# Optimization experiments

Hardware: AMD Instinct MI355X
Metric: run time of the kernel (lower is better)

The kernel has to match this reference:

```python
import jax, jax.numpy as jnp
import numpy as np

N, IN_DIM, HEADS, OUT_DIM = 4096, 128, 4, 64
NEG_INF = -9.0e15  # finite mask value, matches torch source


def setup_inputs() -> dict:
    key = jax.random.key(0)
    k1, k2, k3, k4, k5 = jax.random.split(key, 5)
    x = jax.random.normal(k1, (N, IN_DIM), dtype=jnp.float32)
    adj_mask = jax.random.bernoulli(k2, 0.1, (N, N))  # bool, j->i edges
    # xavier-uniform-ish scales
    lim_w = float(np.sqrt(6.0 / (IN_DIM + HEADS * OUT_DIM)))
    W_lin = jax.random.uniform(k3, (IN_DIM, HEADS * OUT_DIM), minval=-lim_w, maxval=lim_w, dtype=jnp.float32)
    lim_a = float(np.sqrt(6.0 / (2 * OUT_DIM + 1)))
    a_src = jax.random.uniform(k4, (OUT_DIM,), minval=-lim_a, maxval=lim_a, dtype=jnp.float32)
    a_dst = jax.random.uniform(k5, (OUT_DIM,), minval=-lim_a, maxval=lim_a, dtype=jnp.float32)
    return {"x": x, "adj_mask": adj_mask, "W_lin": W_lin, "a_src": a_src, "a_dst": a_dst}


def reference(x, adj_mask, W_lin, a_src, a_dst):
    n = x.shape[0]
    h = (x @ W_lin).reshape(n, HEADS, OUT_DIM)           # (N, H, D)
    # att(cat(h_i, h_j)) decomposes linearly: a_src.h_i + a_dst.h_j
    s_i = jnp.einsum("nhd,d->nh", h, a_src)              # (N, H) contribution of dest node i
    s_j = jnp.einsum("nhd,d->nh", h, a_dst)              # (N, H) contribution of source node j
    e = jax.nn.leaky_relu(s_i[:, None, :] + s_j[None, :, :], 0.2)  # (N, N, H)
    e = jnp.where(adj_mask[:, :, None], e, NEG_INF)
    attn = jax.nn.softmax(e, axis=1)                     # softmax over source nodes j
    out = jnp.einsum("ijh,jhd->ihd", attn, h)            # per-head aggregation
    return out.reshape(n, HEADS * OUT_DIM)               # concat=True
```

## Files before the change

### kernel.cpp

```cpp
#include <hip/hip_runtime.h>
#include <math.h>


#define N 4096
#define IN_DIM 128
#define HEADS 4
#define OUT_DIM 64
#define HD 256
#define LOG2E 1.4426950408889634f

typedef _Float16 f16x8 __attribute__((ext_vector_type(8)));
typedef __fp16 fp16x2 __attribute__((ext_vector_type(2)));
typedef float f32x4 __attribute__((ext_vector_type(4)));

union F16x8u { fp16x2 h2[4]; f16x8 v; };

#define WS_HB_OFF    0u
#define WS_SSRC_OFF  2097152u
#define WS_SDST_OFF  2162688u
#define WS_SDT_OFF   2228224u
#define WS_L2L_OFF   2293760u
#define WS_U_OFF     2359296u
#define WS_BITS_OFF  2424832u
#define WS_BITT_OFF  4521984u
#define WS_PART_OFF  6619136u
#define WS_NEEDED    (6619136u + 33554432u)

__device__ __forceinline__ float f4get(float4 v, int h) {
  return h == 0 ? v.x : h == 1 ? v.y : h == 2 ? v.z : v.w;
}
__device__ __forceinline__ float lrelu(float v) { return fmaxf(v, 0.2f * v); }

__device__ __forceinline__ unsigned pack_bytes(unsigned v) {
  return (v & 1u) | ((v >> 7) & 2u) | ((v >> 14) & 4u) | ((v >> 21) & 8u);
}

__global__ __launch_bounds__(256) void pack_mask_k(const void* __restrict__ mraw,
                                                   unsigned* __restrict__ bits,
                                                   unsigned* __restrict__ bits_t) {
  __shared__ int s_flag;
  if (threadIdx.x == 0) s_flag = 0;
  __syncthreads();
  const unsigned* mw = (const unsigned*)mraw;
  int bad = 0, g = 0;
  for (int i = threadIdx.x; i < 1024; i += 256) {
    unsigned v = mw[i];
    if (v & 0xFEFEFEFEu) bad = 1;
    if (v > 1u) g = 1;
  }
  if (bad || g) atomicOr(&s_flag, (bad ? 1 : 0) | (g ? 2 : 0));
  __syncthreads();
  const bool byte_fmt = ((s_flag & 1) == 0) && ((s_flag & 2) != 0);

  int w = blockIdx.x * blockDim.x + threadIdx.x;
  unsigned ob = 0u;
  if (byte_fmt) {
    const uint4* p = (const uint4*)((const unsigned char*)mraw + (size_t)w * 32u);
    uint4 a = p[0], b = p[1];
    ob  =  pack_bytes(a.x)        | (pack_bytes(a.y) << 4)  | (pack_bytes(a.z) << 8)  | (pack_bytes(a.w) << 12);
    ob |= (pack_bytes(b.x) << 16) | (pack_bytes(b.y) << 20) | (pack_bytes(b.z) << 24) | (pack_bytes(b.w) << 28);
  } else {
    const uint4* p = (const uint4*)((const unsigned*)mraw + (size_t)w * 32u);
#pragma unroll
    for (int k = 0; k < 8; ++k) {
      uint4 v = p[k];
      ob |= (v.x ? 1u : 0u) << (4 * k);
      ob |= (v.y ? 1u : 0u) << (4 * k + 1);
      ob |= (v.z ? 1u : 0u) << (4 * k + 2);
      ob |= (v.w ? 1u : 0u) << (4 * k + 3);
    }
  }
  bits[w] = ob;
  const int row = w >> 7, jc = w & 127;
  bits_t[((size_t)(row >> 6) * 128 + jc) * 64 + (row & 63)] = ob;
}

__global__ __launch_bounds__(256) void compute_h(const float* __restrict__ x,
                                                 const float* __restrict__ W,
                                                 const float* __restrict__ a_src,
                                                 const float* __restrict__ a_dst,
                                                 _Float16* __restrict__ hb,
                                                 float* __restrict__ s_src,
                                                 float* __restrict__ s_dst,
                                                 float* __restrict__ s_dst_t) {
  const int i0 = blockIdx.x * 8;
  const int c = threadIdx.x;

  float acc[8];
#pragma unroll
  for (int r = 0; r < 8; ++r) acc[r] = 0.f;

  for (int kk = 0; kk < IN_DIM / 4; ++kk) {
    const int k = kk * 4;
    float w0 = W[(size_t)(k + 0) * HD + c];
    float w1 = W[(size_t)(k + 1) * HD + c];
    float w2 = W[(size_t)(k + 2) * HD + c];
    float w3 = W[(size_t)(k + 3) * HD + c];
#pragma unroll
    for (int r = 0; r < 8; ++r) {
      float4 xv = *(const float4*)(x + (size_t)(i0 + r) * IN_DIM + k);
      acc[r] = fmaf(xv.x, w0, fmaf(xv.y, w1, fmaf(xv.z, w2, fmaf(xv.w, w3, acc[r]))));
    }
  }

  {
    const int head = c >> 6, nt = (c >> 4) & 3, m15 = c & 15;
    const int unit = (head * 128 + (i0 >> 5)) * 4 + nt;
    const int lanep = ((i0 & 31) >> 3) * 16 + m15;
    f16x8 v;
#pragma unroll
    for (int r = 0; r < 8; ++r) v[r] = (_Float16)acc[r];
    *(f16x8*)(hb + (size_t)unit * 512 + lanep * 8) = v;
  }

  const int hw = c >> 6, lane = c & 63;
  const float as = a_src[lane], ad = a_dst[lane];
#pragma unroll
  for (int r = 0; r < 8; ++r) {
    float vs = acc[r] * as, vd = acc[r] * ad;
#pragma unroll
    for (int off = 1; off < 64; off <<= 1) {
      vs += __shfl_xor(vs, off);
      vd += __shfl_xor(vd, off);
    }
    if (lane == 0) {
      s_src[(size_t)(i0 + r) * HEADS + hw] = vs * LOG2E;
      s_dst[(size_t)(i0 + r) * HEADS + hw] = vd * LOG2E;
      s_dst_t[(size_t)hw * N + (i0 + r)] = vd * LOG2E;
    }
  }
}

__global__ __launch_bounds__(256) void gat_scores(const float* __restrict__ s_src,
                                                  const float* __restrict__ s_dst,
                                                  const unsigned* __restrict__ bits,
                                                  float* __restrict__ log2l_ws,
                                                  float* __restrict__ U_ws) {
  const int tid = threadIdx.x;
  const int wave = tid >> 6;
  const int lane = tid & 63;
  const int row = blockIdx.x * 4 + wave;

  const float4* sd4 = (const float4*)s_dst;
  const unsigned long long* mb64 = (const unsigned long long*)bits + (size_t)row * 64;

  float4 siv = ((const float4*)s_src)[row];
  float si[4] = {siv.x, siv.y, siv.z, siv.w};
  float l[4] = {0.f, 0.f, 0.f, 0.f};

  for (int jb = 0; jb < N / 256; ++jb) {
    float4 sj[4];
    unsigned long long w[4];
#pragma unroll
    for (int u = 0; u < 4; ++u) {
      sj[u] = sd4[jb * 256 + u * 64 + lane];
      w[u] = mb64[jb * 4 + u];
    }
#pragma unroll
    for (int u = 0; u < 4; ++u) {
      bool e = (w[u] >> lane) & 1ull;
#pragma unroll
      for (int h = 0; h < 4; ++h) {
        float ev = __builtin_amdgcn_exp2f(lrelu(si[h] + f4get(sj[u], h)));
        l[h] += e ? ev : 0.f;
      }
    }
  }
#pragma unroll
  for (int off = 1; off < 64; off <<= 1)
#pragma unroll
    for (int h = 0; h < 4; ++h) l[h] += __shfl_xor(l[h], off);

  if (lane == 0) {
#pragma unroll
    for (int h = 0; h < 4; ++h) {
      bool empty = (l[h] == 0.f);
      log2l_ws[(size_t)row * HEADS + h] = empty ? 12.0f : __log2f(l[h]);
      U_ws[(size_t)row * HEADS + h] = empty ? 0.f : -1.0e38f;
    }
  }
}

__global__ __launch_bounds__(512, 4) void gat_aggr(const _Float16* __restrict__ hb,
                                                   const float* __restrict__ s_src,
                                                   const float* __restrict__ s_dst_t,
                                                   const float* __restrict__ log2l_ws,
                                                   const float* __restrict__ U_ws,
                                                   const unsigned* __restrict__ bits_t,
                                                   float* __restrict__ dst,
                                                   int atomic_mode) {
  const int tid = threadIdx.x;
  const int wave = tid >> 6;
  const int lane = tid & 63;
  const int head = wave & 3;
  const int mg = wave >> 2;
  const int m15 = lane & 15;
  const int quad = lane >> 4;
  const int jq = blockIdx.x & 7;
  const int it = blockIdx.x >> 3;
  const int i0 = it * 64;
  const int rA = i0 + mg * 32 + m15;
  const int rB = rA + 16;

  const float siA = s_src[(size_t)rA * HEADS + head];
  const float siB = s_src[(size_t)rB * HEADS + head];
  const float nlA = -log2l_ws[(size_t)rA * HEADS + head];
  const float nlB = -log2l_ws[(size_t)rB * HEADS + head];
  const float UA = U_ws[(size_t)rA * HEADS + head];
  const float UB = U_ws[(size_t)rB * HEADS + head];

  const unsigned* mt = bits_t + ((size_t)it * 128 + jq * 16) * 64 + mg * 32 + m15;
  const float* sjb = s_dst_t + (size_t)head * N + jq * 512 + quad * 8;
  const _Float16* hbp = hb + ((size_t)(head * 128 + jq * 16) * 4) * 512 + lane * 8;

  f32x4 accA0 = {0.f, 0.f, 0.f, 0.f}, accA1 = accA0, accA2 = accA0, accA3 = accA0;
  f32x4 accB0 = accA0, accB1 = accA0, accB2 = accA0, accB3 = accA0;

  const int shq = quad * 8;

  for (int c = 0; c < 16; ++c) {
    const unsigned mwA = mt[c * 64];
    const unsigned mwB = mt[c * 64 + 16];
    const float4 sa = *(const float4*)(sjb + c * 32);
    const float4 sb = *(const float4*)(sjb + c * 32 + 4);

    const f16x8 b0 = *(const f16x8*)(hbp + (size_t)(c * 4 + 0) * 512);
    const f16x8 b1 = *(const f16x8*)(hbp + (size_t)(c * 4 + 1) * 512);
    const f16x8 b2 = *(const f16x8*)(hbp + (size_t)(c * 4 + 2) * 512);
    const f16x8 b3 = *(const f16x8*)(hbp + (size_t)(c * 4 + 3) * 512);

    const unsigned wA = mwA >> shq;
    const unsigned wB = mwB >> shq;
    const float sjs[8] = {sa.x, sa.y, sa.z, sa.w, sb.x, sb.y, sb.z, sb.w};

    F16x8u uA, uB;
#pragma unroll
    for (int t2 = 0; t2 < 4; ++t2) {
      float pA[2], pB[2];
#pragma unroll
      for (int q = 0; q < 2; ++q) {
        const int t = t2 * 2 + q;
        const float sj = sjs[t];
        float vA = lrelu(siA + sj);
        float vB = lrelu(siB + sj);
        float xA = ((wA >> t) & 1u) ? vA : UA;
        float xB = ((wB >> t) & 1u) ? vB : UB;
        pA[q] = __builtin_amdgcn_exp2f(xA + nlA);
        pB[q] = __builtin_amdgcn_exp2f(xB + nlB);
      }
      uA.h2[t2] = __builtin_amdgcn_cvt_pkrtz(pA[0], pA[1]);
      uB.h2[t2] = __builtin_amdgcn_cvt_pkrtz(pB[0], pB[1]);
    }

    accA0 = __builtin_amdgcn_mfma_f32_16x16x32_f16(uA.v, b0, accA0, 0, 0, 0);
    accA1 = __builtin_amdgcn_mfma_f32_16x16x32_f16(uA.v, b1, accA1, 0, 0, 0);
    accA2 = __builtin_amdgcn_mfma_f32_16x16x32_f16(uA.v, b2, accA2, 0, 0, 0);
    accA3 = __builtin_amdgcn_mfma_f32_16x16x32_f16(uA.v, b3, accA3, 0, 0, 0);
    accB0 = __builtin_amdgcn_mfma_f32_16x16x32_f16(uB.v, b0, accB0, 0, 0, 0);
    accB1 = __builtin_amdgcn_mfma_f32_16x16x32_f16(uB.v, b1, accB1, 0, 0, 0);
    accB2 = __builtin_amdgcn_mfma_f32_16x16x32_f16(uB.v, b2, accB2, 0, 0, 0);
    accB3 = __builtin_amdgcn_mfma_f32_16x16x32_f16(uB.v, b3, accB3, 0, 0, 0);
  }

  const int colb = head * 64 + m15;
  if (atomic_mode) {
    float* oA = dst + (size_t)(i0 + mg * 32 + quad * 4) * HD + colb;
    float* oB = oA + (size_t)16 * HD;
#pragma unroll
    for (int reg = 0; reg < 4; ++reg) {
      atomicAdd(oA + (size_t)reg * HD + 0,  accA0[reg]);
      atomicAdd(oA + (size_t)reg * HD + 16, accA1[reg]);
      atomicAdd(oA + (size_t)reg * HD + 32, accA2[reg]);
      atomicAdd(oA + (size_t)reg * HD + 48, accA3[reg]);
      atomicAdd(oB + (size_t)reg * HD + 0,  accB0[reg]);
      atomicAdd(oB + (size_t)reg * HD + 16, accB1[reg]);
      atomicAdd(oB + (size_t)reg * HD + 32, accB2[reg]);
      atomicAdd(oB + (size_t)reg * HD + 48, accB3[reg]);
    }
  } else {
    float* oA = dst + (size_t)jq * (N * HD) + (size_t)(i0 + mg * 32 + quad * 4) * HD + colb;
    float* oB = oA + (size_t)16 * HD;
#pragma unroll
    for (int reg = 0; reg < 4; ++reg) {
      oA[(size_t)reg * HD + 0]  = accA0[reg];
      oA[(size_t)reg * HD + 16] = accA1[reg];
      oA[(size_t)reg * HD + 32] = accA2[reg];
      oA[(size_t)reg * HD + 48] = accA3[reg];
      oB[(size_t)reg * HD + 0]  = accB0[reg];
      oB[(size_t)reg * HD + 16] = accB1[reg];
      oB[(size_t)reg * HD + 32] = accB2[reg];
      oB[(size_t)reg * HD + 48] = accB3[reg];
    }
  }
}

__global__ __launch_bounds__(256) void reduce_part(const float4* __restrict__ part,
                                                   float4* __restrict__ out) {
  const size_t idx = (size_t)blockIdx.x * 256 + threadIdx.x;
  const size_t S = (size_t)N * HD / 4;
  float4 o = part[idx];
#pragma unroll
  for (int k = 1; k < 8; ++k) {
    float4 a = part[idx + (size_t)k * S];
    o.x += a.x; o.y += a.y; o.z += a.z; o.w += a.w;
  }
  out[idx] = o;
}

extern "C" void kernel_launch(void* const* d_in, const int* in_sizes, int n_in,
                              void* d_out, int out_size, void* d_ws, size_t ws_size,
                              hipStream_t stream) {
  (void)in_sizes; (void)n_in;
  const float* x = (const float*)d_in[0];
  const void* mask = d_in[1];
  const float* W = (const float*)d_in[2];
  const float* a_src = (const float*)d_in[3];
  const float* a_dst = (const float*)d_in[4];
  float* out = (float*)d_out;

  char* ws = (char*)d_ws;
  _Float16* hb = (_Float16*)(ws + WS_HB_OFF);
  float* s_src = (float*)(ws + WS_SSRC_OFF);
  float* s_dst = (float*)(ws + WS_SDST_OFF);
  float* s_dst_t = (float*)(ws + WS_SDT_OFF);
  float* log2l_ws = (float*)(ws + WS_L2L_OFF);
  float* U_ws = (float*)(ws + WS_U_OFF);
  unsigned* bits = (unsigned*)(ws + WS_BITS_OFF);
  unsigned* bits_t = (unsigned*)(ws + WS_BITT_OFF);
  float* partial = (float*)(ws + WS_PART_OFF);

  pack_mask_k<<<(N * N / 32) / 256, 256, 0, stream>>>(mask, bits, bits_t);
  compute_h<<<N / 8, 256, 0, stream>>>(x, W, a_src, a_dst, hb, s_src, s_dst, s_dst_t);
  gat_scores<<<N / 4, 256, 0, stream>>>(s_src, s_dst, bits, log2l_ws, U_ws);

  if (ws_size >= (size_t)WS_NEEDED) {
    gat_aggr<<<(N / 64) * 8, 512, 0, stream>>>(hb, s_src, s_dst_t, log2l_ws, U_ws,
                                               bits_t, partial, 0);
    reduce_part<<<(N * HD / 4) / 256, 256, 0, stream>>>((const float4*)partial, (float4*)out);
  } else {
    (void)hipMemsetAsync(out, 0, (size_t)out_size * sizeof(float), stream);
    gat_aggr<<<(N / 64) * 8, 512, 0, stream>>>(hb, s_src, s_dst_t, log2l_ws, U_ws,
                                               bits_t, out, 1);
  }
}
```

Baseline: 174.0 us.

## Drop separate softmax-denominator pass using fixed shift and deferred normalization

Removes the gat_scores kernel that computed per-row softmax denominators, instead accumulating the denominator inside the aggregation loop with a constant exponent shift and normalizing in the reduce step. It also merges mask packing and the h projection into one launch, drops the row-major mask bit array, and adds a fallback for empty rows using the column mean of h. This saves a full pass over the mask and the score exponentials, at the cost of extra per-element adds and a fixed shift that could overflow or underflow fp16 if scores span a wide range.

```diff
diff --git a/kernel.cpp b/kernel.cpp
--- a/kernel.cpp
+++ b/kernel.cpp
@@ -8,6 +8,7 @@
 #define OUT_DIM 64
 #define HD 256
 #define LOG2E 1.4426950408889634f
+#define PSHIFT 8.0f
 
 typedef _Float16 f16x8 __attribute__((ext_vector_type(8)));
 typedef __fp16 fp16x2 __attribute__((ext_vector_type(2)));
@@ -17,166 +18,117 @@
 
 #define WS_HB_OFF    0u
 #define WS_SSRC_OFF  2097152u
-#define WS_SDST_OFF  2162688u
-#define WS_SDT_OFF   2228224u
-#define WS_L2L_OFF   2293760u
-#define WS_U_OFF     2359296u
-#define WS_BITS_OFF  2424832u
-#define WS_BITT_OFF  4521984u
-#define WS_PART_OFF  6619136u
-#define WS_NEEDED    (6619136u + 33554432u)
-
-__device__ __forceinline__ float f4get(float4 v, int h) {
-  return h == 0 ? v.x : h == 1 ? v.y : h == 2 ? v.z : v.w;
-}
+#define WS_SDT_OFF   2162688u
+#define WS_BITT_OFF  2228224u
+#define WS_HSUM_OFF  4325376u
+#define WS_PL_OFF    4329472u
+#define WS_PART_OFF  5242880u
+#define WS_NEED8     (5242880u + 8u * 4194304u)
+#define WS_NEED2     (5242880u + 2u * 4194304u)
+
 __device__ __forceinline__ float lrelu(float v) { return fmaxf(v, 0.2f * v); }
 
 __device__ __forceinline__ unsigned pack_bytes(unsigned v) {
   return (v & 1u) | ((v >> 7) & 2u) | ((v >> 14) & 4u) | ((v >> 21) & 8u);
 }
 
-__global__ __launch_bounds__(256) void pack_mask_k(const void* __restrict__ mraw,
-                                                   unsigned* __restrict__ bits,
-                                                   unsigned* __restrict__ bits_t) {
-  __shared__ int s_flag;
-  if (threadIdx.x == 0) s_flag = 0;
-  __syncthreads();
-  const unsigned* mw = (const unsigned*)mraw;
-  int bad = 0, g = 0;
-  for (int i = threadIdx.x; i < 1024; i += 256) {
-    unsigned v = mw[i];
-    if (v & 0xFEFEFEFEu) bad = 1;
-    if (v > 1u) g = 1;
-  }
-  if (bad || g) atomicOr(&s_flag, (bad ? 1 : 0) | (g ? 2 : 0));
-  __syncthreads();
-  const bool byte_fmt = ((s_flag & 1) == 0) && ((s_flag & 2) != 0);
-
-  int w = blockIdx.x * blockDim.x + threadIdx.x;
-  unsigned ob = 0u;
-  if (byte_fmt) {
-    const uint4* p = (const uint4*)((const unsigned char*)mraw + (size_t)w * 32u);
-    uint4 a = p[0], b = p[1];
-    ob  =  pack_bytes(a.x)        | (pack_bytes(a.y) << 4)  | (pack_bytes(a.z) << 8)  | (pack_bytes(a.w) << 12);
-    ob |= (pack_bytes(b.x) << 16) | (pack_bytes(b.y) << 20) | (pack_bytes(b.z) << 24) | (pack_bytes(b.w) << 28);
+__global__ __launch_bounds__(256) void prep_k(const void* __restrict__ mraw,
+                                              unsigned* __restrict__ bits_t,
+                                              const float* __restrict__ x,
+                                              const float* __restrict__ W,
+                                              const float* __restrict__ a_src,
+                                              const float* __restrict__ a_dst,
+                                              _Float16* __restrict__ hb,
+                                              float* __restrict__ s_src,
+                                              float* __restrict__ s_dst_t,
+                                              float* __restrict__ hsum) {
+  if (blockIdx.x < 2048) {
+    __shared__ int s_flag;
+    if (threadIdx.x == 0) s_flag = 0;
+    __syncthreads();
+    const unsigned* mw = (const unsigned*)mraw;
+    int bad = 0, g = 0;
+    for (int i = threadIdx.x; i < 1024; i += 256) {
+      unsigned v = mw[i];
+      if (v & 0xFEFEFEFEu) bad = 1;
+      if (v > 1u) g = 1;
+    }
+    if (bad || g) atomicOr(&s_flag, (bad ? 1 : 0) | (g ? 2 : 0));
+    __syncthreads();
+    const bool byte_fmt = ((s_flag & 1) == 0) && ((s_flag & 2) != 0);
+
+    int w = blockIdx.x * 256 + threadIdx.x;
+    unsigned ob = 0u;
+    if (byte_fmt) {
+      const uint4* p = (const uint4*)((const unsigned char*)mraw + (size_t)w * 32u);
+      uint4 a = p[0], b = p[1];
+      ob  =  pack_bytes(a.x)        | (pack_bytes(a.y) << 4)  | (pack_bytes(a.z) << 8)  | (pack_bytes(a.w) << 12);
+      ob |= (pack_bytes(b.x) << 16) | (pack_bytes(b.y) << 20) | (pack_bytes(b.z) << 24) | (pack_bytes(b.w) << 28);
+    } else {
+      const uint4* p = (const uint4*)((const unsigned*)mraw + (size_t)w * 32u);
+#pragma unroll
+      for (int k = 0; k < 8; ++k) {
+        uint4 v = p[k];
+        ob |= (v.x ? 1u : 0u) << (4 * k);
+        ob |= (v.y ? 1u : 0u) << (4 * k + 1);
+        ob |= (v.z ? 1u : 0u) << (4 * k + 2);
+        ob |= (v.w ? 1u : 0u) << (4 * k + 3);
+      }
+    }
+    const int row = w >> 7, jc = w & 127;
+    bits_t[((size_t)(row >> 6) * 128 + jc) * 64 + (row & 63)] = ob;
   } else {
-    const uint4* p = (const uint4*)((const unsigned*)mraw + (size_t)w * 32u);
-#pragma unroll
-    for (int k = 0; k < 8; ++k) {
-      uint4 v = p[k];
-      ob |= (v.x ? 1u : 0u) << (4 * k);
-      ob |= (v.y ? 1u : 0u) << (4 * k + 1);
-      ob |= (v.z ? 1u : 0u) << (4 * k + 2);
-      ob |= (v.w ? 1u : 0u) << (4 * k + 3);
-    }
-  }
-  bits[w] = ob;
-  const int row = w >> 7, jc = w & 127;
-  bits_t[((size_t)(row >> 6) * 128 + jc) * 64 + (row & 63)] = ob;
-}
-
-__global__ __launch_bounds__(256) void compute_h(const float* __restrict__ x,
-                                                 const float* __restrict__ W,
-                                                 const float* __restrict__ a_src,
-                                                 const float* __restrict__ a_dst,
-                                                 _Float16* __restrict__ hb,
-                                                 float* __restrict__ s_src,
-                                                 float* __restrict__ s_dst,
-                                                 float* __restrict__ s_dst_t) {
-  const int i0 = blockIdx.x * 8;
-  const int c = threadIdx.x;
-
-  float acc[8];
-#pragma unroll
-  for (int r = 0; r < 8; ++r) acc[r] = 0.f;
-
-  for (int kk = 0; kk < IN_DIM / 4; ++kk) {
-    const int k = kk * 4;
-    float w0 = W[(size_t)(k + 0) * HD + c];
-    float w1 = W[(size_t)(k + 1) * HD + c];
-    float w2 = W[(size_t)(k + 2) * HD + c];
-    float w3 = W[(size_t)(k + 3) * HD + c];
+    const int i0 = (blockIdx.x - 2048) * 8;
+    const int c = threadIdx.x;
+
+    float acc[8];
+#pragma unroll
+    for (int r = 0; r < 8; ++r) acc[r] = 0.f;
+
+    for (int kk = 0; kk < IN_DIM / 4; ++kk) {
+      const int k = kk * 4;
+      float w0 = W[(size_t)(k + 0) * HD + c];
+      float w1 = W[(size_t)(k + 1) * HD + c];
+      float w2 = W[(size_t)(k + 2) * HD + c];
+      float w3 = W[(size_t)(k + 3) * HD + c];
+#pragma unroll
+      for (int r = 0; r < 8; ++r) {
+        float4 xv = *(const float4*)(x + (size_t)(i0 + r) * IN_DIM + k);
+        acc[r] = fmaf(xv.x, w0, fmaf(xv.y, w1, fmaf(xv.z, w2, fmaf(xv.w, w3, acc[r]))));
+      }
+    }
+
+    {
+      const int head = c >> 6, nt = (c >> 4) & 3, m15 = c & 15;
+      const int unit = (head * 128 + (i0 >> 5)) * 4 + nt;
+      const int lanep = ((i0 & 31) >> 3) * 16 + m15;
+      f16x8 v;
+#pragma unroll
+      for (int r = 0; r < 8; ++r) v[r] = (_Float16)acc[r];
+      *(f16x8*)(hb + (size_t)unit * 512 + lanep * 8) = v;
+    }
+
+    {
+      float loc = 0.f;
+#pragma unroll
+      for (int r = 0; r < 8; ++r) loc += acc[r];
+      atomicAdd(&hsum[c], loc);
+    }
+
+    const int hw = c >> 6, lane = c & 63;
+    const float as = a_src[lane], ad = a_dst[lane];
 #pragma unroll
     for (int r = 0; r < 8; ++r) {
-      float4 xv = *(const float4*)(x + (size_t)(i0 + r) * IN_DIM + k);
-      acc[r] = fmaf(xv.x, w0, fmaf(xv.y, w1, fmaf(xv.z, w2, fmaf(xv.w, w3, acc[r]))));
-    }
-  }
-
-  {
-    const int head = c >> 6, nt = (c >> 4) & 3, m15 = c & 15;
-    const int unit = (head * 128 + (i0 >> 5)) * 4 + nt;
-    const int lanep = ((i0 & 31) >> 3) * 16 + m15;
-    f16x8 v;
-#pragma unroll
-    for (int r = 0; r < 8; ++r) v[r] = (_Float16)acc[r];
-    *(f16x8*)(hb + (size_t)unit * 512 + lanep * 8) = v;
-  }
-
-  const int hw = c >> 6, lane = c & 63;
-  const float as = a_src[lane], ad = a_dst[lane];
-#pragma unroll
-  for (int r = 0; r < 8; ++r) {
-    float vs = acc[r] * as, vd = acc[r] * ad;
-#pragma unroll
-    for (int off = 1; off < 64; off <<= 1) {
-      vs += __shfl_xor(vs, off);
-      vd += __shfl_xor(vd, off);
-    }
-    if (lane == 0) {
-      s_src[(size_t)(i0 + r) * HEADS + hw] = vs * LOG2E;
-      s_dst[(size_t)(i0 + r) * HEADS + hw] = vd * LOG2E;
-      s_dst_t[(size_t)hw * N + (i0 + r)] = vd * LOG2E;
-    }
-  }
-}
-
-__global__ __launch_bounds__(256) void gat_scores(const float* __restrict__ s_src,
-                                                  const float* __restrict__ s_dst,
-                                                  const unsigned* __restrict__ bits,
-                                                  float* __restrict__ log2l_ws,
-                                                  float* __restrict__ U_ws) {
-  const int tid = threadIdx.x;
-  const int wave = tid >> 6;
-  const int lane = tid & 63;
-  const int row = blockIdx.x * 4 + wave;
-
-  const float4* sd4 = (const float4*)s_dst;
-  const unsigned long long* mb64 = (const unsigned long long*)bits + (size_t)row * 64;
-
-  float4 siv = ((const float4*)s_src)[row];
-  float si[4] = {siv.x, siv.y, siv.z, siv.w};
-  float l[4] = {0.f, 0.f, 0.f, 0.f};
-
-  for (int jb = 0; jb < N / 256; ++jb) {
-    float4 sj[4];
-    unsigned long long w[4];
-#pragma unroll
-    for (int u = 0; u < 4; ++u) {
-      sj[u] = sd4[jb * 256 + u * 64 + lane];
-      w[u] = mb64[jb * 4 + u];
-    }
-#pragma unroll
-    for (int u = 0; u < 4; ++u) {
-      bool e = (w[u] >> lane) & 1ull;
-#pragma unroll
-      for (int h = 0; h < 4; ++h) {
-        float ev = __builtin_amdgcn_exp2f(lrelu(si[h] + f4get(sj[u], h)));
-        l[h] += e ? ev : 0.f;
-      }
-    }
-  }
-#pragma unroll
-  for (int off = 1; off < 64; off <<= 1)
-#pragma unroll
-    for (int h = 0; h < 4; ++h) l[h] += __shfl_xor(l[h], off);
-
-  if (lane == 0) {
-#pragma unroll
-    for (int h = 0; h < 4; ++h) {
-      bool empty = (l[h] == 0.f);
-      log2l_ws[(size_t)row * HEADS + h] = empty ? 12.0f : __log2f(l[h]);
-      U_ws[(size_t)row * HEADS + h] = empty ? 0.f : -1.0e38f;
+      float vs = acc[r] * as, vd = acc[r] * ad;
+#pragma unroll
+      for (int off = 1; off < 64; off <<= 1) {
+        vs += __shfl_xor(vs, off);
+        vd += __shfl_xor(vd, off);
+      }
+      if (lane == 0) {
+        s_src[(size_t)(i0 + r) * HEADS + hw] = vs * LOG2E;
+        s_dst_t[(size_t)hw * N + (i0 + r)] = vd * LOG2E;
+      }
     }
   }
 }
@@ -184,11 +136,13 @@
 __global__ __launch_bounds__(512, 4) void gat_aggr(const _Float16* __restrict__ hb,
                                                    const float* __restrict__ s_src,
                                                    const float* __restrict__ s_dst_t,
-                                                   const float* __restrict__ log2l_ws,
-                                                   const float* __restrict__ U_ws,
                                                    const unsigned* __restrict__ bits_t,
-                                                   float* __restrict__ dst,
-                                                   int atomic_mode) {
+                                                   float* __restrict__ accp,
+                                                   float* __restrict__ lp,
+                                                   int jshift) {
+  const int jsplit = 1 << jshift;
+  const int jrange = N >> jshift;
+  const int chunks = jrange >> 5;
   const int tid = threadIdx.x;
   const int wave = tid >> 6;
   const int lane = tid & 63;
@@ -196,29 +150,26 @@
   const int mg = wave >> 2;
   const int m15 = lane & 15;
   const int quad = lane >> 4;
-  const int jq = blockIdx.x & 7;
-  const int it = blockIdx.x >> 3;
+  const int jq = blockIdx.x & (jsplit - 1);
+  const int it = blockIdx.x >> jshift;
   const int i0 = it * 64;
   const int rA = i0 + mg * 32 + m15;
   const int rB = rA + 16;
 
   const float siA = s_src[(size_t)rA * HEADS + head];
   const float siB = s_src[(size_t)rB * HEADS + head];
-  const float nlA = -log2l_ws[(size_t)rA * HEADS + head];
-  const float nlB = -log2l_ws[(size_t)rB * HEADS + head];
-  const float UA = U_ws[(size_t)rA * HEADS + head];
-  const float UB = U_ws[(size_t)rB * HEADS + head];
-
-  const unsigned* mt = bits_t + ((size_t)it * 128 + jq * 16) * 64 + mg * 32 + m15;
-  const float* sjb = s_dst_t + (size_t)head * N + jq * 512 + quad * 8;
-  const _Float16* hbp = hb + ((size_t)(head * 128 + jq * 16) * 4) * 512 + lane * 8;
+
+  const unsigned* mt = bits_t + ((size_t)it * 128 + jq * chunks) * 64 + mg * 32 + m15;
+  const float* sjb = s_dst_t + (size_t)head * N + jq * jrange + quad * 8;
+  const _Float16* hbp = hb + ((size_t)(head * 128 + jq * chunks) * 4) * 512 + lane * 8;
 
   f32x4 accA0 = {0.f, 0.f, 0.f, 0.f}, accA1 = accA0, accA2 = accA0, accA3 = accA0;
   f32x4 accB0 = accA0, accB1 = accA0, accB2 = accA0, accB3 = accA0;
+  float lA = 0.f, lB = 0.f;
 
   const int shq = quad * 8;
 
-  for (int c = 0; c < 16; ++c) {
+  for (int c = 0; c < chunks; ++c) {
     const unsigned mwA = mt[c * 64];
     const unsigned mwB = mt[c * 64 + 16];
     const float4 sa = *(const float4*)(sjb + c * 32);
@@ -243,10 +194,12 @@
         const float sj = sjs[t];
         float vA = lrelu(siA + sj);
         float vB = lrelu(siB + sj);
-        float xA = ((wA >> t) & 1u) ? vA : UA;
-        float xB = ((wB >> t) & 1u) ? vB : UB;
-        pA[q] = __builtin_amdgcn_exp2f(xA + nlA);
-        pB[q] = __builtin_amdgcn_exp2f(xB + nlB);
+        float xA = (((wA >> t) & 1u) ? vA : -1.0e38f) - PSHIFT;
+        float xB = (((wB >> t) & 1u) ? vB : -1.0e38f) - PSHIFT;
+        pA[q] = __builtin_amdgcn_exp2f(xA);
+        pB[q] = __builtin_amdgcn_exp2f(xB);
+        lA += pA[q];
+        lB += pB[q];
       }
       uA.h2[t2] = __builtin_amdgcn_cvt_pkrtz(pA[0], pA[1]);
       uB.h2[t2] = __builtin_amdgcn_cvt_pkrtz(pB[0], pB[1]);
@@ -262,47 +215,53 @@
     accB3 = __builtin_amdgcn_mfma_f32_16x16x32_f16(uB.v, b3, accB3, 0, 0, 0);
   }
 
+  lA += __shfl_xor(lA, 16); lA += __shfl_xor(lA, 32);
+  lB += __shfl_xor(lB, 16); lB += __shfl_xor(lB, 32);
+  if (quad == 0) {
+    lp[((size_t)jq * N + rA) * HEADS + head] = lA;
+    lp[((size_t)jq * N + rB) * HEADS + head] = lB;
+  }
+
   const int colb = head * 64 + m15;
-  if (atomic_mode) {
-    float* oA = dst + (size_t)(i0 + mg * 32 + quad * 4) * HD + colb;
-    float* oB = oA + (size_t)16 * HD;
-#pragma unroll
-    for (int reg = 0; reg < 4; ++reg) {
-      atomicAdd(oA + (size_t)reg * HD + 0,  accA0[reg]);
-      atomicAdd(oA + (size_t)reg * HD + 16, accA1[reg]);
-      atomicAdd(oA + (size_t)reg * HD + 32, accA2[reg]);
-      atomicAdd(oA + (size_t)reg * HD + 48, accA3[reg]);
-      atomicAdd(oB + (size_t)reg * HD + 0,  accB0[reg]);
-      atomicAdd(oB + (size_t)reg * HD + 16, accB1[reg]);
-      atomicAdd(oB + (size_t)reg * HD + 32, accB2[reg]);
-      atomicAdd(oB + (size_t)reg * HD + 48, accB3[reg]);
-    }
+  float* oA = accp + (size_t)jq * (N * HD) + (size_t)(i0 + mg * 32 + quad * 4) * HD + colb;
+  float* oB = oA + (size_t)16 * HD;
+#pragma unroll
+  for (int reg = 0; reg < 4; ++reg) {
+    oA[(size_t)reg * HD + 0]  = accA0[reg];
+    oA[(size_t)reg * HD + 16] = accA1[reg];
+    oA[(size_t)reg * HD + 32] = accA2[reg];
+    oA[(size_t)reg * HD + 48] = accA3[reg];
+    oB[(size_t)reg * HD + 0]  = accB0[reg];
+    oB[(size_t)reg * HD + 16] = accB1[reg];
+    oB[(size_t)reg * HD + 32] = accB2[reg];
+    oB[(size_t)reg * HD + 48] = accB3[reg];
+  }
+}
+
+__global__ __launch_bounds__(256) void reduce_part(const float4* __restrict__ accp,
+                                                   const float* __restrict__ lp,
+                                                   const float* __restrict__ hsum,
+                                                   float4* __restrict__ out, int jsplit) {
+  const size_t idx = (size_t)blockIdx.x * 256 + threadIdx.x;
+  const int row = (int)(idx >> 6);
+  const int col4 = (int)(idx & 63);
+  const int head = col4 >> 4;
+  const size_t S = (size_t)N * HD / 4;
+
+  float4 o = accp[idx];
+  float lt = lp[(size_t)row * HEADS + head];
+  for (int k = 1; k < jsplit; ++k) {
+    float4 a = accp[idx + (size_t)k * S];
+    o.x += a.x; o.y += a.y; o.z += a.z; o.w += a.w;
+    lt += lp[((size_t)k * N + row) * HEADS + head];
+  }
+  if (lt == 0.f) {
+    float4 hs = ((const float4*)hsum)[col4];
+    const float c = 1.0f / (float)N;
+    o.x = hs.x * c; o.y = hs.y * c; o.z = hs.z * c; o.w = hs.w * c;
   } else {
-    float* oA = dst + (size_t)jq * (N * HD) + (size_t)(i0 + mg * 32 + quad * 4) * HD + colb;
-    float* oB = oA + (size_t)16 * HD;
-#pragma unroll
-    for (int reg = 0; reg < 4; ++reg) {
-      oA[(size_t)reg * HD + 0]  = accA0[reg];
-      oA[(size_t)reg * HD + 16] = accA1[reg];
-      oA[(size_t)reg * HD + 32] = accA2[reg];
-      oA[(size_t)reg * HD + 48] = accA3[reg];
-      oB[(size_t)reg * HD + 0]  = accB0[reg];
-      oB[(size_t)reg * HD + 16] = accB1[reg];
-      oB[(size_t)reg * HD + 32] = accB2[reg];
-      oB[(size_t)reg * HD + 48] = accB3[reg];
-    }
-  }
-}
-
-__global__ __launch_bounds__(256) void reduce_part(const float4* __restrict__ part,
-                                                   float4* __restrict__ out) {
-  const size_t idx = (size_t)blockIdx.x * 256 + threadIdx.x;
-  const size_t S = (size_t)N * HD / 4;
-  float4 o = part[idx];
-#pragma unroll
-  for (int k = 1; k < 8; ++k) {
-    float4 a = part[idx + (size_t)k * S];
-    o.x += a.x; o.y += a.y; o.z += a.z; o.w += a.w;
+    const float inv = 1.0f / lt;
+    o.x *= inv; o.y *= inv; o.z *= inv; o.w *= inv;
   }
   out[idx] = o;
 }
@@ -310,7 +269,7 @@
 extern "C" void kernel_launch(void* const* d_in, const int* in_sizes, int n_in,
                               void* d_out, int out_size, void* d_ws, size_t ws_size,
                               hipStream_t stream) {
-  (void)in_sizes; (void)n_in;
+  (void)in_sizes; (void)n_in; (void)out_size;
   const float* x = (const float*)d_in[0];
   const void* mask = d_in[1];
   const float* W = (const float*)d_in[2];
@@ -321,25 +280,20 @@
   char* ws = (char*)d_ws;
   _Float16* hb = (_Float16*)(ws + WS_HB_OFF);
   float* s_src = (float*)(ws + WS_SSRC_OFF);
-  float* s_dst = (float*)(ws + WS_SDST_OFF);
   float* s_dst_t = (float*)(ws + WS_SDT_OFF);
-  float* log2l_ws = (float*)(ws + WS_L2L_OFF);
-  float* U_ws = (float*)(ws + WS_U_OFF);
-  unsigned* bits = (unsigned*)(ws + WS_BITS_OFF);
   unsigned* bits_t = (unsigned*)(ws + WS_BITT_OFF);
-  float* partial = (float*)(ws + WS_PART_OFF);
-
-  pack_mask_k<<<(N * N / 32) / 256, 256, 0, stream>>>(mask, bits, bits_t);
-  compute_h<<<N / 8, 256, 0, stream>>>(x, W, a_src, a_dst, hb, s_src, s_dst, s_dst_t);
-  gat_scores<<<N / 4, 256, 0, stream>>>(s_src, s_dst, bits, log2l_ws, U_ws);
-
-  if (ws_size >= (size_t)WS_NEEDED) {
-    gat_aggr<<<(N / 64) * 8, 512, 0, stream>>>(hb, s_src, s_dst_t, log2l_ws, U_ws,
-                                               bits_t, partial, 0);
-    reduce_part<<<(N * HD / 4) / 256, 256, 0, stream>>>((const float4*)partial, (float4*)out);
-  } else {
-    (void)hipMemsetAsync(out, 0, (size_t)out_size * sizeof(float), stream);
-    gat_aggr<<<(N / 64) * 8, 512, 0, stream>>>(hb, s_src, s_dst_t, log2l_ws, U_ws,
-                                               bits_t, out, 1);
-  }
-}
+  float* hsum = (float*)(ws + WS_HSUM_OFF);
+  float* lp = (float*)(ws + WS_PL_OFF);
+  float* accp = (float*)(ws + WS_PART_OFF);
+
+  const int jshift = (ws_size >= (size_t)WS_NEED8) ? 3 : 1;
+  const int jsplit = 1 << jshift;
+
+  (void)hipMemsetAsync(hsum, 0, HD * sizeof(float), stream);
+  prep_k<<<2048 + N / 8, 256, 0, stream>>>(mask, bits_t, x, W, a_src, a_dst,
+                                           hb, s_src, s_dst_t, hsum);
+  gat_aggr<<<(N / 64) * jsplit, 512, 0, stream>>>(hb, s_src, s_dst_t, bits_t,
+                                                  accp, lp, jshift);
+  reduce_part<<<(N * HD / 4) / 256, 256, 0, stream>>>((const float4*)accp, lp, hsum,
+                                                      (float4*)out, jsplit);
+}
```

Result: faster. 163.5 us (-6.0%).
